# Optimization experiments

Measured on AMD Instinct MI355X. Metric: run time of the kernel, lower is better.

The kernel has to match this reference:

```python
import jax, jax.numpy as jnp
import numpy as np


def mish(x):
    return x * jnp.tanh(jax.nn.softplus(x))


def gcn(x, W, b, src, dst):
    # PyG GCNConv: h = D^-1/2 (A+I) D^-1/2 (x W) + b, aggregation at dst=edge_index[1]
    n = x.shape[0]
    h = x @ W
    deg = jax.ops.segment_sum(jnp.ones(src.shape[0], x.dtype), dst, num_segments=n) + 1.0
    dinv = jax.lax.rsqrt(deg)
    msg = h[src] * (dinv[src] * dinv[dst])[:, None]
    agg = jax.ops.segment_sum(msg, dst, num_segments=n)
    return agg + h * (dinv * dinv)[:, None] + b


def pool_mean(x, seg, num_segments):
    s = jax.ops.segment_sum(x, seg, num_segments=num_segments)
    c = jax.ops.segment_sum(jnp.ones(x.shape[0], x.dtype), seg, num_segments=num_segments)
    return s / jnp.maximum(c, 1.0)[:, None]


def attention(x, qW, qb, kW, kb, vW, vb, G):
    # x: [G*R, in_feats] -> per-graph self-attention over ROIs (dropout is identity in eval)
    R = x.shape[0] // G
    xc = x.reshape(G, R, x.shape[1])
    Q = xc @ qW + qb
    K = xc @ kW + kb
    Vv = xc @ vW + vb
    scores = jnp.einsum('gqd,gkd->gqk', Q, K) / (Q.shape[-1] ** 0.5)
    w = jax.nn.softmax(scores, axis=-1)
    out = jnp.einsum('gqk,gkd->gqd', w, Vv).reshape(G * R, Vv.shape[-1])
    return out, w.mean(axis=0)


def closs(a, b, temp=0.6):
    a = a / jnp.maximum(jnp.linalg.norm(a, axis=1, keepdims=True), 1e-12)
    b = b / jnp.maximum(jnp.linalg.norm(b, axis=1, keepdims=True), 1e-12)
    logits = (a @ b.T) / temp
    return -jnp.mean(jnp.diagonal(jax.nn.log_softmax(logits, axis=1)))


def setup_inputs() -> dict:
    key = jax.random.key(0)
    G, R1, R2, F_IN, H, OUT, DEG, V = 512, 200, 160, 128, 64, 64, 16, 64
    N1, N2 = G * R1, G * R2
    ks = iter(jax.random.split(key, 64))
    d = {}
    d['x1'] = jax.random.normal(next(ks), (N1, R1 + 3), jnp.float32)
    d['x2'] = jax.random.normal(next(ks), (N2, R2 + 3), jnp.float32)

    def lin(name, i, o):
        d[name + '_W'] = jax.random.normal(next(ks), (i, o), jnp.float32) * (i ** -0.5)
        d[name + '_b'] = jnp.zeros((o,), jnp.float32)

    lin('fcl', R1 + 3, F_IN); lin('fcr', R2 + 3, F_IN)
    lin('fcl1', R1, F_IN); lin('fcr1', R2, F_IN)
    lin('a1_q', F_IN, OUT); lin('a1_k', F_IN, OUT); lin('a1_v', F_IN, OUT)
    lin('a2_q', F_IN, OUT); lin('a2_k', F_IN, OUT); lin('a2_v', F_IN, OUT)
    lin('conv', F_IN, H); lin('conv1', H, H)
    lin('mlp', H, OUT)
    lin('fc1a', OUT * 4, F_IN); lin('fc1b', F_IN, 2)

    def edges(k, R):
        k1, k2 = jax.random.split(k)
        off = (jnp.arange(G, dtype=jnp.int32) * R)[:, None]
        src = jax.random.randint(k1, (G, R * DEG), 0, R, jnp.int32) + off
        dst = jax.random.randint(k2, (G, R * DEG), 0, R, jnp.int32) + off
        return jnp.stack([src.reshape(-1), dst.reshape(-1)])

    d['edge_index1'] = edges(next(ks), R1)
    d['edge_index2'] = edges(next(ks), R2)
    d['batch1'] = jnp.repeat(jnp.arange(G, dtype=jnp.int32), R1)
    d['batch2'] = jnp.repeat(jnp.arange(G, dtype=jnp.int32), R2)

    def sub(k, R):
        # one visited-node set (as in RW_subgraph) tiled per graph with offsets
        vis = jnp.sort(jax.random.permutation(k, R)[:V]).astype(jnp.int32)
        return (vis[None, :] + (jnp.arange(G, dtype=jnp.int32) * R)[:, None]).reshape(-1)

    d['sub_idx1'] = sub(next(ks), R1)
    d['sub_idx2'] = sub(next(ks), R2)
    d['num_graphs'] = G
    return d


def reference(x1, x2, fcl_W, fcl_b, fcr_W, fcr_b, fcl1_W, fcl1_b, fcr1_W, fcr1_b,
              a1_q_W, a1_q_b, a1_k_W, a1_k_b, a1_v_W, a1_v_b,
              a2_q_W, a2_q_b, a2_k_W, a2_k_b, a2_v_W, a2_v_b,
              conv_W, conv_b, conv1_W, conv1_b, mlp_W, mlp_b,
              fc1a_W, fc1a_b, fc1b_W, fc1b_b,
              edge_index1, edge_index2, batch1, batch2, sub_idx1, sub_idx2, num_graphs):
    G = int(num_graphs)
    src1, dst1 = edge_index1[0], edge_index1[1]
    src2, dst2 = edge_index2[0], edge_index2[1]

    z1 = x1[:, :-3] @ fcl1_W + fcl1_b
    z2 = x2[:, :-3] @ fcr1_W + fcr1_b
    z1, aw1 = attention(z1, a1_q_W, a1_q_b, a1_k_W, a1_k_b, a1_v_W, a1_v_b, G)
    z2, aw2 = attention(z2, a2_q_W, a2_q_b, a2_k_W, a2_k_b, a2_v_W, a2_v_b, G)
    z1 = pool_mean(z1, batch1, G)
    z2 = pool_mean(z2, batch2, G)

    h1 = x1 @ fcl_W + fcl_b
    h2 = x2 @ fcr_W + fcr_b
    o1 = mish(gcn(h1, conv_W, conv_b, src1, dst1))
    o2 = mish(gcn(h2, conv_W, conv_b, src2, dst2))
    o1 = gcn(o1, conv1_W, conv1_b, src1, dst1)
    o2 = gcn(o2, conv1_W, conv1_b, src2, dst2)

    s1 = o1[sub_idx1] @ mlp_W + mlp_b
    s2 = o2[sub_idx2] @ mlp_W + mlp_b
    s1 = pool_mean(s1, batch1[sub_idx1], G)
    s2 = pool_mean(s2, batch2[sub_idx2], G)

    c_loss = closs(s1, z2) + closs(z1, s2)
    feat = jnp.concatenate([s1, z1, s2, z2], axis=1)
    out = mish(feat @ fc1a_W + fc1a_b) @ fc1b_W + fc1b_b
    return c_loss, out, aw1, aw2
```

## Files before the change

### kernel.cpp

```cpp
#include <hip/hip_runtime.h>
#include <math.h>

#define TPB 256
#define MAXR 200
#define MAXEP 4608

typedef float f32x4 __attribute__((ext_vector_type(4)));
typedef __bf16 bfv8 __attribute__((ext_vector_type(8)));

union U8 { uint4 q; unsigned short us[8]; __bf16 b[8]; bfv8 v; };

__device__ __forceinline__ unsigned short f2bfu(float f) {
  union { __bf16 h; unsigned short u; } x;
  x.h = (__bf16)f;
  return x.u;
}
__device__ __forceinline__ float bfu2f(unsigned short u) {
  return __uint_as_float((unsigned)u << 16);
}

__device__ __forceinline__ float mish_f(float x) {
  float sp = fmaxf(x, 0.f) + log1pf(expf(-fabsf(x)));
  return x * tanhf(sp);
}

__device__ __forceinline__ U8 loadA_f32(const float* Af, int kb, int K, bool rowok) {
  U8 u;
  if (rowok && kb + 8 <= K) {
    float4 f0 = *(const float4*)(Af + kb);
    float4 f1 = *(const float4*)(Af + kb + 4);
    u.b[0]=(__bf16)f0.x; u.b[1]=(__bf16)f0.y; u.b[2]=(__bf16)f0.z; u.b[3]=(__bf16)f0.w;
    u.b[4]=(__bf16)f1.x; u.b[5]=(__bf16)f1.y; u.b[6]=(__bf16)f1.z; u.b[7]=(__bf16)f1.w;
  } else {
#pragma unroll
    for (int j = 0; j < 8; ++j) {
      float f = (rowok && kb + j < K) ? Af[kb + j] : 0.f;
      u.b[j] = (__bf16)f;
    }
  }
  return u;
}

template<bool ABF16, bool CBF16, bool MISH, int NJ, int KPMAX>
__global__ __launch_bounds__(256) void gemm2(
    const void* __restrict__ Av, const unsigned short* __restrict__ Bt,
    const float* __restrict__ bias, void* __restrict__ Cv,
    int N, int M, int K, int lda, int ldc,
    long sA, long sB, long sC, float alpha, int Kpad)
{
  constexpr int BM = NJ * 16;
  __shared__ unsigned short Bs[BM * KPMAX];

  const int tid = threadIdx.x;
  const int col0 = blockIdx.x * BM, row0 = blockIdx.y * 64;

  {
    const unsigned short* Bp = Bt + (long)blockIdx.z * sB + (long)col0 * Kpad;
    int rows = M - col0; if (rows > BM) rows = BM;
    const int total = rows * Kpad;
    for (int i = tid * 8; i < total; i += TPB * 32) {
      uint4 a0, a1, a2, a3;
      bool b1 = i + TPB * 8  < total;
      bool b2 = i + TPB * 16 < total;
      bool b3 = i + TPB * 24 < total;
      a0 = *(const uint4*)&Bp[i];
      if (b1) a1 = *(const uint4*)&Bp[i + TPB * 8];
      if (b2) a2 = *(const uint4*)&Bp[i + TPB * 16];
      if (b3) a3 = *(const uint4*)&Bp[i + TPB * 24];
      *(uint4*)&Bs[i] = a0;
      if (b1) *(uint4*)&Bs[i + TPB * 8]  = a1;
      if (b2) *(uint4*)&Bs[i + TPB * 16] = a2;
      if (b3) *(uint4*)&Bs[i + TPB * 24] = a3;
    }
  }

  const int lane = tid & 63, w = tid >> 6;
  const int mrow = lane & 15, kg = lane >> 4;
  const int arow = row0 + w * 16 + mrow;
  const bool rowok = arow < N;

  const unsigned short* Ah = nullptr;
  const float* Af = nullptr;
  if (ABF16) Ah = (const unsigned short*)Av + (long)blockIdx.z * sA + (long)arow * lda;
  else       Af = (const float*)Av + (long)blockIdx.z * sA + (long)arow * lda;

  U8 ua;
  if (ABF16) ua.q = *(const uint4*)(Ah + kg * 8);
  else       ua   = loadA_f32(Af, kg * 8, K, rowok);

  __syncthreads();

  f32x4 acc[NJ];
#pragma unroll
  for (int j = 0; j < NJ; ++j) acc[j] = (f32x4)0.f;

  for (int k0 = 0; k0 < K; k0 += 32) {
    U8 un;
    bool more = (k0 + 32) < K;
    if (more) {
      if (ABF16) un.q = *(const uint4*)(Ah + k0 + 32 + kg * 8);
      else       un   = loadA_f32(Af, k0 + 32 + kg * 8, K, rowok);
    }
    const int kb = k0 + kg * 8;
#pragma unroll
    for (int j = 0; j < NJ; ++j) {
      U8 ub;
      ub.q = *(const uint4*)&Bs[(j * 16 + mrow) * Kpad + kb];
      acc[j] = __builtin_amdgcn_mfma_f32_16x16x32_bf16(ua.v, ub.v, acc[j], 0, 0, 0);
    }
    if (more) ua = un;
  }

  long cbase = (long)blockIdx.z * sC;
#pragma unroll
  for (int j = 0; j < NJ; ++j) {
    int gc = col0 + j * 16 + mrow;
    if (gc >= M) continue;
    float bb = bias ? bias[gc] : 0.f;
#pragma unroll
    for (int r = 0; r < 4; ++r) {
      int gr = row0 + w * 16 + kg * 4 + r;
      if (gr >= N) continue;
      float v = acc[j][r] * alpha + bb;
      if (MISH) v = mish_f(v);
      if (CBF16) ((unsigned short*)Cv)[cbase + (long)gr * ldc + gc] = f2bfu(v);
      else       ((float*)Cv)[cbase + (long)gr * ldc + gc] = v;
    }
  }
}

static inline int kpad_of(int K) { return ((K + 31) / 32) * 32 + 8; }

struct PrepSeg { const float* src; void* dst; int K, M, Kpad, kind; };
struct PrepArgs { PrepSeg s[19]; };

__global__ __launch_bounds__(256) void prep_weights(PrepArgs a) {
  PrepSeg sg = a.s[blockIdx.x];
  if (sg.kind == 0) {
    unsigned short* d = (unsigned short*)sg.dst;
    int tot = sg.M * sg.Kpad;
    for (int i = threadIdx.x; i < tot; i += TPB) {
      int m = i / sg.Kpad, k = i - m * sg.Kpad;
      float f = (k < sg.K) ? sg.src[(long)k * sg.M + m] : 0.f;
      d[i] = f2bfu(f);
    }
  } else {
    float* d = (float*)sg.dst;
    for (int i = threadIdx.x; i < sg.K; i += TPB) d[i] = sg.src[i];
  }
}

__global__ __launch_bounds__(256) void xcast(const float* __restrict__ x,
                                             unsigned short* __restrict__ xb,
                                             int C, int S)
{
  long r0 = (long)blockIdx.x * 8;
  for (int i = threadIdx.x; i < 8 * S; i += TPB) {
    int rr = i / S, c = i - rr * S;
    long r = r0 + rr;
    xb[r * S + c] = f2bfu(c < C ? x[r * C + c] : 0.f);
  }
}

__global__ __launch_bounds__(256) void ktvt_kernel(
    const unsigned short* __restrict__ QKV, unsigned short* __restrict__ Kt,
    unsigned short* __restrict__ Vt, int R, int Rpad)
{
  int g = blockIdx.x;
  const unsigned short* q = QKV + (long)g * R * 192;
  unsigned short* kt = Kt + (long)g * R * 72;
  unsigned short* vt = Vt + (long)g * 64 * Rpad;
  int c = threadIdx.x & 63, w = threadIdx.x >> 6;
  for (int r = w; r < R; r += 4) {
    kt[r * 72 + c] = q[(long)r * 192 + 64 + c];
    vt[c * Rpad + r] = q[(long)r * 192 + 128 + c];
  }
  int pad = Rpad - R;
  for (int i = threadIdx.x; i < 64 * pad; i += TPB) {
    int cc = i / pad, k = i - cc * pad;
    vt[cc * Rpad + R + k] = 0;
  }
}

__global__ __launch_bounds__(256) void adj_build(
    const int* __restrict__ src, const int* __restrict__ dst,
    unsigned short* __restrict__ Adj, int R, int Rpad, int EPG)
{
  __shared__ float dinv_s[256];
  __shared__ unsigned short ssrc[MAXEP];
  __shared__ int cnt[256];
  __shared__ int scan[256];
  __shared__ int offx[257];
  __shared__ int cur[256];
  __shared__ float rowbuf[4][256];

  int g = blockIdx.x, tid = threadIdx.x;
  long ebase = (long)g * EPG;
  int gR = g * R;

  cnt[tid] = 0;
  __syncthreads();
  for (int e = tid; e < EPG; e += TPB)
    atomicAdd(&cnt[dst[ebase + e] - gR], 1);
  __syncthreads();

  int x = cnt[tid];
  int pc = (x + 7) & ~7;
  scan[tid] = pc;
  __syncthreads();
#pragma unroll
  for (int s = 1; s < 256; s <<= 1) {
    int t = (tid >= s) ? scan[tid - s] : 0;
    __syncthreads();
    scan[tid] += t;
    __syncthreads();
  }
  if (tid == 0) offx[0] = 0;
  offx[tid + 1] = scan[tid];
  cur[tid] = scan[tid] - pc;
  dinv_s[tid] = rsqrtf((float)x + 1.f);
  {
    unsigned dummy2 = 0xFFFFFFFFu;
    for (int i = tid; i < MAXEP / 2; i += TPB) ((unsigned*)ssrc)[i] = dummy2;
  }
  __syncthreads();

  for (int e = tid; e < EPG; e += TPB) {
    int d = dst[ebase + e] - gR;
    int s = src[ebase + e] - gR;
    int pos = atomicAdd(&cur[d], 1);
    ssrc[pos] = (unsigned short)s;
  }
  __syncthreads();

  int lane = tid & 63, w = tid >> 6;
  float* rb = rowbuf[w];
  for (int d = w; d < R; d += 4) {
#pragma unroll
    for (int i = 0; i < 4; ++i) rb[lane + i * 64] = 0.f;
    int i0 = offx[d], i1 = offx[d + 1];
    for (int i = i0 + lane; i < i1; i += 64) {
      int s = ssrc[i];
      if (s < R) atomicAdd(&rb[s], dinv_s[s]);
    }
    float dd = dinv_s[d];
    int c0 = lane * 4;
    if (c0 < Rpad) {
      ushort4 o;
      float v0 = rb[c0]     + (c0     == d ? dd : 0.f);
      float v1 = rb[c0 + 1] + (c0 + 1 == d ? dd : 0.f);
      float v2 = rb[c0 + 2] + (c0 + 2 == d ? dd : 0.f);
      float v3 = rb[c0 + 3] + (c0 + 3 == d ? dd : 0.f);
      o.x = f2bfu(v0 * dd); o.y = f2bfu(v1 * dd);
      o.z = f2bfu(v2 * dd); o.w = f2bfu(v3 * dd);
      *(ushort4*)&Adj[((long)gR + d) * Rpad + c0] = o;
    }
  }
}

__global__ __launch_bounds__(256) void transp64(
    const unsigned short* __restrict__ X, unsigned short* __restrict__ XT,
    int R, int Rpad)
{
  __shared__ unsigned short tile[64][72];
  int g = blockIdx.x, tid = threadIdx.x;
  const unsigned short* xg = X + (long)g * R * 64;
  unsigned short* xt = XT + (long)g * 64 * Rpad;
  for (int r0 = 0; r0 < Rpad; r0 += 64) {
    __syncthreads();
    for (int i = tid; i < 64 * 64; i += TPB) {
      int rr = i >> 6, cc = i & 63;
      int r = r0 + rr;
      tile[cc][rr] = (r < R) ? xg[(long)r * 64 + cc] : (unsigned short)0;
    }
    __syncthreads();
    int c = tid >> 2, j0 = (tid & 3) * 16;
    int lim = Rpad - r0; if (lim > 64) lim = 64;
    for (int jj = j0; jj < j0 + 16 && jj < lim; jj += 8) {
      uint4 q = *(const uint4*)&tile[c][jj];
      *(uint4*)&xt[(long)c * Rpad + r0 + jj] = q;
    }
  }
}

__global__ __launch_bounds__(256) void softmax_bf16(unsigned short* __restrict__ S,
                                                    int R, long rows)
{
  long wid = (long)blockIdx.x * 4 + (threadIdx.x >> 6);
  if (wid >= rows) return;
  int lane = threadIdx.x & 63;
  unsigned short* row = S + wid * R;
  float v[4];
  float mx = -1e30f;
#pragma unroll
  for (int t = 0; t < 4; ++t) {
    int j = lane + t * 64;
    v[t] = (j < R) ? bfu2f(row[j]) : -1e30f;
    mx = fmaxf(mx, v[t]);
  }
#pragma unroll
  for (int o = 32; o; o >>= 1) mx = fmaxf(mx, __shfl_xor(mx, o));
  float s = 0.f;
#pragma unroll
  for (int t = 0; t < 4; ++t) {
    int j = lane + t * 64;
    if (j < R) { v[t] = expf(v[t] - mx); s += v[t]; }
  }
#pragma unroll
  for (int o = 32; o; o >>= 1) s += __shfl_xor(s, o);
  float inv = 1.f / s;
#pragma unroll
  for (int t = 0; t < 4; ++t) {
    int j = lane + t * 64;
    if (j < R) row[j] = f2bfu(v[t] * inv);
  }
}

__global__ void meang_bf16(const unsigned short* __restrict__ S, float* __restrict__ out,
                           int RR, int G, float inv)
{
  int idx = blockIdx.x * TPB + threadIdx.x;
  if (idx >= RR) return;
  const unsigned short* p = S + idx;
  float s = 0.f;
  for (int g = 0; g + 8 <= G; g += 8) {
    s += bfu2f(p[(long)g * RR])       + bfu2f(p[(long)(g + 1) * RR]) +
         bfu2f(p[(long)(g + 2) * RR]) + bfu2f(p[(long)(g + 3) * RR]) +
         bfu2f(p[(long)(g + 4) * RR]) + bfu2f(p[(long)(g + 5) * RR]) +
         bfu2f(p[(long)(g + 6) * RR]) + bfu2f(p[(long)(g + 7) * RR]);
  }
  out[idx] = s * inv;
}

__global__ __launch_bounds__(256) void pool_mean_bf16(const unsigned short* __restrict__ X,
                                                      float* __restrict__ out, int R)
{
  __shared__ float part[4][64];
  int g = blockIdx.x, lane = threadIdx.x & 63, w = threadIdx.x >> 6;
  float s = 0.f;
  for (int r = w; r < R; r += 4)
    s += bfu2f(X[((long)g * R + r) * 64 + lane]);
  part[w][lane] = s;
  __syncthreads();
  if (w == 0)
    out[g * 64 + lane] = (part[0][lane] + part[1][lane] + part[2][lane] + part[3][lane]) * (1.f / R);
}

__global__ __launch_bounds__(64) void sub_mean_kernel(const unsigned short* __restrict__ X,
                                                      const int* __restrict__ sub,
                                                      float* __restrict__ out, int V)
{
  int g = blockIdx.x, lane = threadIdx.x;
  float s = 0.f;
  for (int v = 0; v + 4 <= V; v += 4) {
    int i0 = sub[g * V + v],     i1 = sub[g * V + v + 1];
    int i2 = sub[g * V + v + 2], i3 = sub[g * V + v + 3];
    s += bfu2f(X[(long)i0 * 64 + lane]) + bfu2f(X[(long)i1 * 64 + lane]) +
         bfu2f(X[(long)i2 * 64 + lane]) + bfu2f(X[(long)i3 * 64 + lane]);
  }
  out[g * 64 + lane] = s * (1.f / V);
}

__global__ __launch_bounds__(64) void norm_rows_kernel(const float* __restrict__ X,
                                                       float* __restrict__ Y)
{
  int g = blockIdx.x, lane = threadIdx.x;
  float x = X[g * 64 + lane];
  float ss = x * x;
#pragma unroll
  for (int o = 32; o; o >>= 1) ss += __shfl_xor(ss, o);
  float n = fmaxf(sqrtf(ss), 1e-12f);
  Y[g * 64 + lane] = x / n;
}

__global__ __launch_bounds__(256) void closs_kernel(const float* __restrict__ An,
                                                    const float* __restrict__ Bn,
                                                    float* __restrict__ loss, int G,
                                                    float invTemp, float coef)
{
  int i = blockIdx.x;
  __shared__ float arow[64];
  __shared__ float logits[512];
  __shared__ float red[256];
  int t = threadIdx.x;
  if (t < 64) arow[t] = An[i * 64 + t];
  __syncthreads();
  for (int j = t; j < G; j += 256) {
    const float* bp = Bn + (long)j * 64;
    float d = 0.f;
#pragma unroll
    for (int k = 0; k < 64; ++k) d = fmaf(arow[k], bp[k], d);
    logits[j] = d * invTemp;
  }
  __syncthreads();
  float mx = -1e30f;
  for (int j = t; j < G; j += 256) mx = fmaxf(mx, logits[j]);
  red[t] = mx; __syncthreads();
  for (int o = 128; o; o >>= 1) { if (t < o) red[t] = fmaxf(red[t], red[t + o]); __syncthreads(); }
  mx = red[0]; __syncthreads();
  float s = 0.f;
  for (int j = t; j < G; j += 256) s += expf(logits[j] - mx);
  red[t] = s; __syncthreads();
  for (int o = 128; o; o >>= 1) { if (t < o) red[t] += red[t + o]; __syncthreads(); }
  if (t == 0) {
    float lse = mx + logf(red[0]);
    atomicAdd(loss, coef * (lse - logits[i]));
  }
}

__global__ __launch_bounds__(128) void head_kernel(
    const float* __restrict__ s1, const float* __restrict__ z1,
    const float* __restrict__ s2, const float* __restrict__ z2,
    const float* __restrict__ W1, const float* __restrict__ b1,
    const float* __restrict__ W2, const float* __restrict__ b2,
    float* __restrict__ out)
{
  int g = blockIdx.x, t = threadIdx.x;
  __shared__ float feat[256];
  __shared__ float hid[128];
  if (t < 64) {
    feat[t]       = s1[g * 64 + t];
    feat[64 + t]  = z1[g * 64 + t];
    feat[128 + t] = s2[g * 64 + t];
    feat[192 + t] = z2[g * 64 + t];
  }
  __syncthreads();
  float acc = b1[t];
  for (int k = 0; k < 256; ++k) acc = fmaf(feat[k], W1[k * 128 + t], acc);
  hid[t] = mish_f(acc);
  __syncthreads();
  if (t < 2) {
    float a2 = b2[t];
#pragma unroll
    for (int k = 0; k < 128; ++k) a2 = fmaf(hid[k], W2[k * 2 + t], a2);
    out[g * 2 + t] = a2;
  }
}

#define LAUNCH_GEMM(ABF,CBF,MISH,NJ,KP, A,B,BI,C, N,M,K,LDA,LDC,SA,SB,SC,BAT,AL,KPAD) \
  { dim3 g_(((M)+(NJ)*16-1)/((NJ)*16), ((N)+63)/64, (BAT)); \
    gemm2<ABF,CBF,MISH,NJ,KP><<<g_,256,0,stream>>>((A),(B),(BI),(C),(N),(M),(K),(LDA),(LDC),(SA),(SB),(SC),(AL),(KPAD)); }

extern "C" void kernel_launch(void* const* d_in, const int* in_sizes, int n_in,
                              void* d_out, int out_size, void* d_ws, size_t ws_size,
                              hipStream_t stream)
{
  const float* x1     = (const float*)d_in[0];
  const float* x2     = (const float*)d_in[1];
  const float* fcl_W  = (const float*)d_in[2];  const float* fcl_b  = (const float*)d_in[3];
  const float* fcr_W  = (const float*)d_in[4];  const float* fcr_b  = (const float*)d_in[5];
  const float* fcl1_W = (const float*)d_in[6];  const float* fcl1_b = (const float*)d_in[7];
  const float* fcr1_W = (const float*)d_in[8];  const float* fcr1_b = (const float*)d_in[9];
  const float* a1qW = (const float*)d_in[10]; const float* a1qb = (const float*)d_in[11];
  const float* a1kW = (const float*)d_in[12]; const float* a1kb = (const float*)d_in[13];
  const float* a1vW = (const float*)d_in[14]; const float* a1vb = (const float*)d_in[15];
  const float* a2qW = (const float*)d_in[16]; const float* a2qb = (const float*)d_in[17];
  const float* a2kW = (const float*)d_in[18]; const float* a2kb = (const float*)d_in[19];
  const float* a2vW = (const float*)d_in[20]; const float* a2vb = (const float*)d_in[21];
  const float* convW  = (const float*)d_in[22]; const float* convb  = (const float*)d_in[23];
  const float* conv1W = (const float*)d_in[24]; const float* conv1b = (const float*)d_in[25];
  const float* mlpW   = (const float*)d_in[26]; const float* mlpb   = (const float*)d_in[27];
  const float* fc1aW  = (const float*)d_in[28]; const float* fc1ab  = (const float*)d_in[29];
  const float* fc1bW  = (const float*)d_in[30]; const float* fc1bb  = (const float*)d_in[31];
  const int* ei1  = (const int*)d_in[32];
  const int* ei2  = (const int*)d_in[33];
  const int* sub1 = (const int*)d_in[36];
  const int* sub2 = (const int*)d_in[37];

  const int R1 = in_sizes[6] / 128;
  const int R2 = in_sizes[8] / 128;
  const int N1 = in_sizes[34];
  const int N2 = in_sizes[35];
  const int G  = N1 / R1;
  const int E1 = in_sizes[32] / 2, E2 = in_sizes[33] / 2;
  const int EPG1 = E1 / G, EPG2 = E2 / G;
  const int V = in_sizes[36] / G;

  const int XS = 232;
  const int Kp1  = kpad_of(R1);
  const int Kp2  = kpad_of(R2);
  const int Kp1f = kpad_of(R1 + 3);
  const int Kp2f = kpad_of(R2 + 3);
  const int Rpad1 = Kp1, Rpad2 = Kp2;

  char* wp = (char*)d_ws;
  auto alloc = [&](size_t bytes) -> char* {
    char* p = wp; wp += (bytes + 255) & ~(size_t)255; return p;
  };
  unsigned short* x1b = (unsigned short*)alloc((size_t)N1 * XS * 2);
  unsigned short* x2b = (unsigned short*)alloc((size_t)N2 * XS * 2);
  size_t raSh = (size_t)G * R1 * R1;
  if ((size_t)N1 * 128 > raSh) raSh = (size_t)N1 * 128;
  unsigned short* RA = (unsigned short*)alloc(raSh * 2);
  unsigned short* RB = (unsigned short*)alloc((size_t)N1 * 192 * 2);
  unsigned short* Kt = (unsigned short*)alloc((size_t)G * R1 * 72 * 2);
  unsigned short* Vt = (unsigned short*)alloc((size_t)G * 64 * Rpad1 * 2);
  unsigned short* W5 = (unsigned short*)alloc((size_t)N1 * 64 * 2);
  unsigned short* fcl1t  = (unsigned short*)alloc((size_t)128 * Kp1 * 2);
  unsigned short* fcr1t  = (unsigned short*)alloc((size_t)128 * Kp2 * 2);
  unsigned short* fclt   = (unsigned short*)alloc((size_t)128 * Kp1f * 2);
  unsigned short* fcrt   = (unsigned short*)alloc((size_t)128 * Kp2f * 2);
  unsigned short* Wc1t   = (unsigned short*)alloc((size_t)192 * 136 * 2);
  unsigned short* Wc2t   = (unsigned short*)alloc((size_t)192 * 136 * 2);
  unsigned short* convt  = (unsigned short*)alloc((size_t)64 * 136 * 2);
  unsigned short* conv1t = (unsigned short*)alloc((size_t)64 * 72 * 2);
  unsigned short* mlpt   = (unsigned short*)alloc((size_t)64 * 72 * 2);
  float* bc1 = (float*)alloc(192 * 4);
  float* bc2 = (float*)alloc(192 * 4);
  float* Pz1 = (float*)alloc((size_t)G * 64 * 4);
  float* Pz2 = (float*)alloc((size_t)G * 64 * 4);
  float* Ps1 = (float*)alloc((size_t)G * 64 * 4);
  float* Ps2 = (float*)alloc((size_t)G * 64 * 4);
  float* Mt  = (float*)alloc((size_t)G * 64 * 4);
  float* n_s1 = (float*)alloc((size_t)G * 64 * 4);
  float* n_z2 = (float*)alloc((size_t)G * 64 * 4);
  float* n_z1 = (float*)alloc((size_t)G * 64 * 4);
  float* n_s2 = (float*)alloc((size_t)G * 64 * 4);
  (void)alloc(4096);

  unsigned short* Adj1 = x1b;
  unsigned short* Adj2 = x2b;

  float* loss = (float*)d_out;
  float* outp = loss + 1;
  float* aw1  = outp + (size_t)G * 2;
  float* aw2  = aw1 + (size_t)R1 * R1;

  hipMemsetAsync(d_out, 0, sizeof(float), stream);

  PrepArgs pa;
  int seg = 0;
  auto addp = [&](const float* s, unsigned short* d, int K, int M, int Kp) {
    pa.s[seg].src = s; pa.s[seg].dst = d; pa.s[seg].K = K; pa.s[seg].M = M;
    pa.s[seg].Kpad = Kp; pa.s[seg].kind = 0; seg++;
  };
  auto addb = [&](const float* s, float* d, int n) {
    pa.s[seg].src = s; pa.s[seg].dst = d; pa.s[seg].K = n; pa.s[seg].M = 0;
    pa.s[seg].Kpad = 0; pa.s[seg].kind = 1; seg++;
  };
  addp(fcl1_W, fcl1t, R1, 128, Kp1);
  addp(fcr1_W, fcr1t, R2, 128, Kp2);
  addp(fcl_W,  fclt,  R1 + 3, 128, Kp1f);
  addp(fcr_W,  fcrt,  R2 + 3, 128, Kp2f);
  addp(a1qW, Wc1t,             128, 64, 136);
  addp(a1kW, Wc1t + 64 * 136,  128, 64, 136);
  addp(a1vW, Wc1t + 128 * 136, 128, 64, 136);
  addp(a2qW, Wc2t,             128, 64, 136);
  addp(a2kW, Wc2t + 64 * 136,  128, 64, 136);
  addp(a2vW, Wc2t + 128 * 136, 128, 64, 136);
  addp(convW,  convt,  128, 64, 136);
  addp(conv1W, conv1t, 64, 64, 72);
  addp(mlpW,   mlpt,   64, 64, 72);
  addb(a1qb, bc1, 64); addb(a1kb, bc1 + 64, 64); addb(a1vb, bc1 + 128, 64);
  addb(a2qb, bc2, 64); addb(a2kb, bc2 + 64, 64); addb(a2vb, bc2 + 128, 64);
  prep_weights<<<seg, 256, 0, stream>>>(pa);

  xcast<<<N1 / 8, 256, 0, stream>>>(x1, x1b, R1 + 3, XS);
  xcast<<<N2 / 8, 256, 0, stream>>>(x2, x2b, R2 + 3, XS);

  LAUNCH_GEMM(true, true, false, 8, 232, x1b, fcl1t, fcl1_b, RA,
              N1, 128, R1, XS, 128, 0, 0, 0, 1, 1.f, Kp1);
  LAUNCH_GEMM(true, true, false, 12, 136, RA, Wc1t, bc1, RB,
              N1, 192, 128, 128, 192, 0, 0, 0, 1, 1.f, 136);
  ktvt_kernel<<<G, 256, 0, stream>>>(RB, Kt, Vt, R1, Rpad1);
  LAUNCH_GEMM(true, true, false, 8, 72, RB, Kt, nullptr, RA,
              R1, R1, 64, 192, R1, (long)R1 * 192, (long)R1 * 72, (long)R1 * R1,
              G, 0.125f, 72);
  {
    long rows = (long)G * R1;
    softmax_bf16<<<(int)((rows + 3) / 4), 256, 0, stream>>>(RA, R1, rows);
    meang_bf16<<<(R1 * R1 + TPB - 1) / TPB, TPB, 0, stream>>>(RA, aw1, R1 * R1, G, 1.f / G);
  }
  LAUNCH_GEMM(true, true, false, 4, 232, RA, Vt, nullptr, W5,
              R1, 64, R1, R1, 64, (long)R1 * R1, (long)64 * Rpad1, (long)R1 * 64,
              G, 1.f, Rpad1);
  pool_mean_bf16<<<G, 256, 0, stream>>>(W5, Pz1, R1);

  LAUNCH_GEMM(true, true, false, 8, 232, x2b, fcr1t, fcr1_b, RA,
              N2, 128, R2, XS, 128, 0, 0, 0, 1, 1.f, Kp2);
  LAUNCH_GEMM(true, true, false, 12, 136, RA, Wc2t, bc2, RB,
              N2, 192, 128, 128, 192, 0, 0, 0, 1, 1.f, 136);
  ktvt_kernel<<<G, 256, 0, stream>>>(RB, Kt, Vt, R2, Rpad2);
  LAUNCH_GEMM(true, true, false, 8, 72, RB, Kt, nullptr, RA,
              R2, R2, 64, 192, R2, (long)R2 * 192, (long)R2 * 72, (long)R2 * R2,
              G, 0.125f, 72);
  {
    long rows = (long)G * R2;
    softmax_bf16<<<(int)((rows + 3) / 4), 256, 0, stream>>>(RA, R2, rows);
    meang_bf16<<<(R2 * R2 + TPB - 1) / TPB, TPB, 0, stream>>>(RA, aw2, R2 * R2, G, 1.f / G);
  }
  LAUNCH_GEMM(true, true, false, 4, 232, RA, Vt, nullptr, W5,
              R2, 64, R2, R2, 64, (long)R2 * R2, (long)64 * Rpad2, (long)R2 * 64,
              G, 1.f, Rpad2);
  pool_mean_bf16<<<G, 256, 0, stream>>>(W5, Pz2, R2);

  unsigned short* hW0 = RB;
  unsigned short* hW1 = RB + (size_t)N1 * 64;
  unsigned short* hW2 = RB + (size_t)N1 * 128;
  LAUNCH_GEMM(true, true, false, 8, 232, x1b, fclt, fcl_b, RA,
              N1, 128, R1 + 3, XS, 128, 0, 0, 0, 1, 1.f, Kp1f);
  LAUNCH_GEMM(true, true, false, 4, 136, RA, convt, nullptr, hW0,
              N1, 64, 128, 128, 64, 0, 0, 0, 1, 1.f, 136);
  adj_build<<<G, 256, 0, stream>>>(ei1, ei1 + E1, Adj1, R1, Rpad1, EPG1);
  transp64<<<G, 256, 0, stream>>>(hW0, Vt, R1, Rpad1);
  LAUNCH_GEMM(true, true, true, 4, 232, Adj1, Vt, convb, hW1,
              R1, 64, R1, Rpad1, 64, (long)R1 * Rpad1, (long)64 * Rpad1, (long)R1 * 64,
              G, 1.f, Rpad1);
  LAUNCH_GEMM(true, true, false, 4, 136, hW1, conv1t, nullptr, hW2,
              N1, 64, 64, 64, 64, 0, 0, 0, 1, 1.f, 72);
  transp64<<<G, 256, 0, stream>>>(hW2, Vt, R1, Rpad1);
  LAUNCH_GEMM(true, true, false, 4, 232, Adj1, Vt, conv1b, hW0,
              R1, 64, R1, Rpad1, 64, (long)R1 * Rpad1, (long)64 * Rpad1, (long)R1 * 64,
              G, 1.f, Rpad1);
  sub_mean_kernel<<<G, 64, 0, stream>>>(hW0, sub1, Mt, V);
  LAUNCH_GEMM(false, false, false, 4, 136, Mt, mlpt, mlpb, Ps1,
              G, 64, 64, 64, 64, 0, 0, 0, 1, 1.f, 72);

  LAUNCH_GEMM(true, true, false, 8, 232, x2b, fcrt, fcr_b, RA,
              N2, 128, R2 + 3, XS, 128, 0, 0, 0, 1, 1.f, Kp2f);
  LAUNCH_GEMM(true, true, false, 4, 136, RA, convt, nullptr, hW0,
              N2, 64, 128, 128, 64, 0, 0, 0, 1, 1.f, 136);
  adj_build<<<G, 256, 0, stream>>>(ei2, ei2 + E2, Adj2, R2, Rpad2, EPG2);
  transp64<<<G, 256, 0, stream>>>(hW0, Vt, R2, Rpad2);
  LAUNCH_GEMM(true, true, true, 4, 232, Adj2, Vt, convb, hW1,
              R2, 64, R2, Rpad2, 64, (long)R2 * Rpad2, (long)64 * Rpad2, (long)R2 * 64,
              G, 1.f, Rpad2);
  LAUNCH_GEMM(true, true, false, 4, 136, hW1, conv1t, nullptr, hW2,
              N2, 64, 64, 64, 64, 0, 0, 0, 1, 1.f, 72);
  transp64<<<G, 256, 0, stream>>>(hW2, Vt, R2, Rpad2);
  LAUNCH_GEMM(true, true, false, 4, 232, Adj2, Vt, conv1b, hW0,
              R2, 64, R2, Rpad2, 64, (long)R2 * Rpad2, (long)64 * Rpad2, (long)R2 * 64,
              G, 1.f, Rpad2);
  sub_mean_kernel<<<G, 64, 0, stream>>>(hW0, sub2, Mt, V);
  LAUNCH_GEMM(false, false, false, 4, 136, Mt, mlpt, mlpb, Ps2,
              G, 64, 64, 64, 64, 0, 0, 0, 1, 1.f, 72);

  norm_rows_kernel<<<G, 64, 0, stream>>>(Ps1, n_s1);
  norm_rows_kernel<<<G, 64, 0, stream>>>(Pz2, n_z2);
  norm_rows_kernel<<<G, 64, 0, stream>>>(Pz1, n_z1);
  norm_rows_kernel<<<G, 64, 0, stream>>>(Ps2, n_s2);
  const float invTemp = 1.f / 0.6f;
  closs_kernel<<<G, 256, 0, stream>>>(n_s1, n_z2, loss, G, invTemp, 1.f / G);
  closs_kernel<<<G, 256, 0, stream>>>(n_z1, n_s2, loss, G, invTemp, 1.f / G);

  head_kernel<<<G, 128, 0, stream>>>(Ps1, Pz1, Ps2, Pz2, fc1aW, fc1ab, fc1bW, fc1bb, outp);
}
```

Measured before the change: 1.007 ms.

## Drop fp32-to-bf16 input cast pass and tile V transpose through shared memory

Removes the xcast pre-pass that converted x1/x2 to padded bf16 buffers. The input-projection GEMMs now read the fp32 inputs directly through the GEMM's fp32 A-path, so the extra write and reread of the large inputs is gone. The adjacency matrices get their own workspace allocations because they previously aliased the cast buffers. The K/V transpose kernel now stages V through a shared-memory tile and writes 16-byte vectors instead of scattered 2-byte stores. The trade-off is that the GEMMs load fp32 with an unaligned row stride (R+3) and convert inside the kernel, which may slow their loads.

```diff
diff --git a/kernel.cpp b/kernel.cpp
--- a/kernel.cpp
+++ b/kernel.cpp
@@ -2,7 +2,6 @@
 #include <math.h>
 
 #define TPB 256
-#define MAXR 200
 #define MAXEP 4608
 
 typedef float f32x4 __attribute__((ext_vector_type(4)));
@@ -150,35 +149,36 @@
   }
 }
 
-__global__ __launch_bounds__(256) void xcast(const float* __restrict__ x,
-                                             unsigned short* __restrict__ xb,
-                                             int C, int S)
-{
-  long r0 = (long)blockIdx.x * 8;
-  for (int i = threadIdx.x; i < 8 * S; i += TPB) {
-    int rr = i / S, c = i - rr * S;
-    long r = r0 + rr;
-    xb[r * S + c] = f2bfu(c < C ? x[r * C + c] : 0.f);
-  }
-}
-
-__global__ __launch_bounds__(256) void ktvt_kernel(
+__global__ __launch_bounds__(256) void ktvt2(
     const unsigned short* __restrict__ QKV, unsigned short* __restrict__ Kt,
     unsigned short* __restrict__ Vt, int R, int Rpad)
 {
-  int g = blockIdx.x;
+  __shared__ unsigned short tile[64][72];
+  int g = blockIdx.x, tid = threadIdx.x;
   const unsigned short* q = QKV + (long)g * R * 192;
   unsigned short* kt = Kt + (long)g * R * 72;
   unsigned short* vt = Vt + (long)g * 64 * Rpad;
-  int c = threadIdx.x & 63, w = threadIdx.x >> 6;
-  for (int r = w; r < R; r += 4) {
-    kt[r * 72 + c] = q[(long)r * 192 + 64 + c];
-    vt[c * Rpad + r] = q[(long)r * 192 + 128 + c];
-  }
-  int pad = Rpad - R;
-  for (int i = threadIdx.x; i < 64 * pad; i += TPB) {
-    int cc = i / pad, k = i - cc * pad;
-    vt[cc * Rpad + R + k] = 0;
+
+  {
+    int c = tid & 63, w = tid >> 6;
+    for (int r = w; r < R; r += 4)
+      kt[r * 72 + c] = q[(long)r * 192 + 64 + c];
+  }
+
+  for (int r0 = 0; r0 < Rpad; r0 += 64) {
+    __syncthreads();
+    for (int i = tid; i < 64 * 64; i += TPB) {
+      int rr = i >> 6, cc = i & 63;
+      int r = r0 + rr;
+      tile[cc][rr] = (r < R) ? q[(long)r * 192 + 128 + cc] : (unsigned short)0;
+    }
+    __syncthreads();
+    int c = tid >> 2, j0 = (tid & 3) * 16;
+    int lim = Rpad - r0; if (lim > 64) lim = 64;
+    for (int jj = j0; jj < j0 + 16 && jj < lim; jj += 8) {
+      uint4 qv = *(const uint4*)&tile[c][jj];
+      *(uint4*)&vt[(long)c * Rpad + r0 + jj] = qv;
+    }
   }
 }
 
@@ -476,7 +476,6 @@
   const int EPG1 = E1 / G, EPG2 = E2 / G;
   const int V = in_sizes[36] / G;
 
-  const int XS = 232;
   const int Kp1  = kpad_of(R1);
   const int Kp2  = kpad_of(R2);
   const int Kp1f = kpad_of(R1 + 3);
@@ -487,8 +486,6 @@
   auto alloc = [&](size_t bytes) -> char* {
     char* p = wp; wp += (bytes + 255) & ~(size_t)255; return p;
   };
-  unsigned short* x1b = (unsigned short*)alloc((size_t)N1 * XS * 2);
-  unsigned short* x2b = (unsigned short*)alloc((size_t)N2 * XS * 2);
   size_t raSh = (size_t)G * R1 * R1;
   if ((size_t)N1 * 128 > raSh) raSh = (size_t)N1 * 128;
   unsigned short* RA = (unsigned short*)alloc(raSh * 2);
@@ -496,6 +493,8 @@
   unsigned short* Kt = (unsigned short*)alloc((size_t)G * R1 * 72 * 2);
   unsigned short* Vt = (unsigned short*)alloc((size_t)G * 64 * Rpad1 * 2);
   unsigned short* W5 = (unsigned short*)alloc((size_t)N1 * 64 * 2);
+  unsigned short* Adj1 = (unsigned short*)alloc((size_t)G * R1 * Rpad1 * 2);
+  unsigned short* Adj2 = (unsigned short*)alloc((size_t)G * R2 * Rpad2 * 2);
   unsigned short* fcl1t  = (unsigned short*)alloc((size_t)128 * Kp1 * 2);
   unsigned short* fcr1t  = (unsigned short*)alloc((size_t)128 * Kp2 * 2);
   unsigned short* fclt   = (unsigned short*)alloc((size_t)128 * Kp1f * 2);
@@ -516,10 +515,7 @@
   float* n_z2 = (float*)alloc((size_t)G * 64 * 4);
   float* n_z1 = (float*)alloc((size_t)G * 64 * 4);
   float* n_s2 = (float*)alloc((size_t)G * 64 * 4);
-  (void)alloc(4096);
-
-  unsigned short* Adj1 = x1b;
-  unsigned short* Adj2 = x2b;
+  (void)alloc(65536);
 
   float* loss = (float*)d_out;
   float* outp = loss + 1;
@@ -555,14 +551,11 @@
   addb(a2qb, bc2, 64); addb(a2kb, bc2 + 64, 64); addb(a2vb, bc2 + 128, 64);
   prep_weights<<<seg, 256, 0, stream>>>(pa);
 
-  xcast<<<N1 / 8, 256, 0, stream>>>(x1, x1b, R1 + 3, XS);
-  xcast<<<N2 / 8, 256, 0, stream>>>(x2, x2b, R2 + 3, XS);
-
-  LAUNCH_GEMM(true, true, false, 8, 232, x1b, fcl1t, fcl1_b, RA,
-              N1, 128, R1, XS, 128, 0, 0, 0, 1, 1.f, Kp1);
+  LAUNCH_GEMM(false, true, false, 8, 232, x1, fcl1t, fcl1_b, RA,
+              N1, 128, R1, R1 + 3, 128, 0, 0, 0, 1, 1.f, Kp1);
   LAUNCH_GEMM(true, true, false, 12, 136, RA, Wc1t, bc1, RB,
               N1, 192, 128, 128, 192, 0, 0, 0, 1, 1.f, 136);
-  ktvt_kernel<<<G, 256, 0, stream>>>(RB, Kt, Vt, R1, Rpad1);
+  ktvt2<<<G, 256, 0, stream>>>(RB, Kt, Vt, R1, Rpad1);
   LAUNCH_GEMM(true, true, false, 8, 72, RB, Kt, nullptr, RA,
               R1, R1, 64, 192, R1, (long)R1 * 192, (long)R1 * 72, (long)R1 * R1,
               G, 0.125f, 72);
@@ -576,11 +569,11 @@
               G, 1.f, Rpad1);
   pool_mean_bf16<<<G, 256, 0, stream>>>(W5, Pz1, R1);
 
-  LAUNCH_GEMM(true, true, false, 8, 232, x2b, fcr1t, fcr1_b, RA,
-              N2, 128, R2, XS, 128, 0, 0, 0, 1, 1.f, Kp2);
+  LAUNCH_GEMM(false, true, false, 8, 232, x2, fcr1t, fcr1_b, RA,
+              N2, 128, R2, R2 + 3, 128, 0, 0, 0, 1, 1.f, Kp2);
   LAUNCH_GEMM(true, true, false, 12, 136, RA, Wc2t, bc2, RB,
               N2, 192, 128, 128, 192, 0, 0, 0, 1, 1.f, 136);
-  ktvt_kernel<<<G, 256, 0, stream>>>(RB, Kt, Vt, R2, Rpad2);
+  ktvt2<<<G, 256, 0, stream>>>(RB, Kt, Vt, R2, Rpad2);
   LAUNCH_GEMM(true, true, false, 8, 72, RB, Kt, nullptr, RA,
               R2, R2, 64, 192, R2, (long)R2 * 192, (long)R2 * 72, (long)R2 * R2,
               G, 0.125f, 72);
@@ -597,8 +590,8 @@
   unsigned short* hW0 = RB;
   unsigned short* hW1 = RB + (size_t)N1 * 64;
   unsigned short* hW2 = RB + (size_t)N1 * 128;
-  LAUNCH_GEMM(true, true, false, 8, 232, x1b, fclt, fcl_b, RA,
-              N1, 128, R1 + 3, XS, 128, 0, 0, 0, 1, 1.f, Kp1f);
+  LAUNCH_GEMM(false, true, false, 8, 232, x1, fclt, fcl_b, RA,
+              N1, 128, R1 + 3, R1 + 3, 128, 0, 0, 0, 1, 1.f, Kp1f);
   LAUNCH_GEMM(true, true, false, 4, 136, RA, convt, nullptr, hW0,
               N1, 64, 128, 128, 64, 0, 0, 0, 1, 1.f, 136);
   adj_build<<<G, 256, 0, stream>>>(ei1, ei1 + E1, Adj1, R1, Rpad1, EPG1);
@@ -616,8 +609,8 @@
   LAUNCH_GEMM(false, false, false, 4, 136, Mt, mlpt, mlpb, Ps1,
               G, 64, 64, 64, 64, 0, 0, 0, 1, 1.f, 72);
 
-  LAUNCH_GEMM(true, true, false, 8, 232, x2b, fcrt, fcr_b, RA,
-              N2, 128, R2 + 3, XS, 128, 0, 0, 0, 1, 1.f, Kp2f);
+  LAUNCH_GEMM(false, true, false, 8, 232, x2, fcrt, fcr_b, RA,
+              N2, 128, R2 + 3, R2 + 3, 128, 0, 0, 0, 1, 1.f, Kp2f);
   LAUNCH_GEMM(true, true, false, 4, 136, RA, convt, nullptr, hW0,
               N2, 64, 128, 128, 64, 0, 0, 0, 1, 1.f, 136);
   adj_build<<<G, 256, 0, stream>>>(ei2, ei2 + E2, Adj2, R2, Rpad2, EPG2);
```

Result: faster. 960.8 us (-4.6%).
